# Optimization experiments

Measured on AMD Instinct MI355X. Metric: run time of the kernel, lower is better.

## Reference

```python
import jax, jax.numpy as jnp
import numpy as np

B, S, D_IN, D_HID, D_OUT, H = 2, 2048, 1024, 1024, 1024, 16
HD = D_HID // H  # head_dim = 64


def setup_inputs() -> dict:
    key = jax.random.key(0)
    ks = jax.random.split(key, 9)
    s_in = 1.0 / np.sqrt(D_IN)
    s_out = 1.0 / np.sqrt(D_OUT)
    return {
        "x": jax.random.normal(ks[0], (B, S, D_IN), dtype=jnp.float32),
        "Wq": jax.random.uniform(ks[1], (D_IN, D_HID), jnp.float32, -s_in, s_in),
        "bq": jax.random.uniform(ks[2], (D_HID,), jnp.float32, -s_in, s_in),
        "Wk": jax.random.uniform(ks[3], (D_IN, D_HID), jnp.float32, -s_in, s_in),
        "bk": jax.random.uniform(ks[4], (D_HID,), jnp.float32, -s_in, s_in),
        "Wv": jax.random.uniform(ks[5], (D_IN, D_OUT), jnp.float32, -s_in, s_in),
        "bv": jax.random.uniform(ks[6], (D_OUT,), jnp.float32, -s_in, s_in),
        "Wo": jax.random.uniform(ks[7], (D_OUT, D_OUT), jnp.float32, -s_out, s_out),
        "bo": jax.random.uniform(ks[8], (D_OUT,), jnp.float32, -s_out, s_out),
    }


def reference(x, Wq, bq, Wk, bk, Wv, bv, Wo, bo):
    b, s, _ = x.shape
    q = (x @ Wq + bq).reshape(b, s, H, HD)  # [B,S,H,HD]
    k = (x @ Wk + bk).reshape(b, s, H, HD)
    v = (x @ Wv + bv).reshape(b, s, H, HD)
    scores = jnp.einsum("bqhd,bkhd->bhqk", q, k) / jnp.sqrt(jnp.float32(HD))
    attn = jax.nn.softmax(scores, axis=-1)  # [B,H,S,S]
    ctx = jnp.einsum("bhqk,bkhd->bqhd", attn, v).reshape(b, s, D_HID)
    return ctx @ Wo + bo
```

## Files before the change

### kernel.cpp

```cpp
#include <hip/hip_runtime.h>
#include <stdint.h>

typedef __attribute__((ext_vector_type(8))) short short8v;
typedef __attribute__((ext_vector_type(4))) short short4v;
typedef __attribute__((ext_vector_type(4))) float float4v;
typedef __attribute__((ext_vector_type(4))) unsigned short ushort4v;
typedef __attribute__((ext_vector_type(4))) float floatvec4;
typedef __attribute__((ext_vector_type(2))) unsigned int uint2v;
typedef __attribute__((ext_vector_type(4))) unsigned int uint4v;

#define DEVI __device__ __forceinline__

DEVI unsigned short f2bf(float f) {
    unsigned int u = __builtin_bit_cast(unsigned int, f);
    u += 0x7FFFu + ((u >> 16) & 1u);
    return (unsigned short)(u >> 16);
}

DEVI unsigned int pk2bf(float a, float b) {
#if defined(__has_builtin) && __has_builtin(__builtin_amdgcn_cvt_pk_bf16_f32)
    auto r = __builtin_amdgcn_cvt_pk_bf16_f32(a, b);
    unsigned int u;
    __builtin_memcpy(&u, &r, 4);
    return u;
#else
    return (unsigned int)f2bf(a) | ((unsigned int)f2bf(b) << 16);
#endif
}

DEVI float ex2(float x) {
#if defined(__has_builtin) && __has_builtin(__builtin_amdgcn_exp2f)
    return __builtin_amdgcn_exp2f(x);
#else
    return __builtin_exp2f(x);
#endif
}

DEVI uint2v pl32swap(unsigned int d, unsigned int s) {
#if defined(__has_builtin) && __has_builtin(__builtin_amdgcn_permlane32_swap)
    return __builtin_amdgcn_permlane32_swap(d, s, false, false);
#else
    const int hi = (int)(threadIdx.x & 32);
    unsigned int dp = __shfl_xor(d, 32), sp = __shfl_xor(s, 32);
    return (uint2v){hi ? sp : d, hi ? s : dp};
#endif
}
DEVI uint2v pl16swap(unsigned int d, unsigned int s) {
#if defined(__has_builtin) && __has_builtin(__builtin_amdgcn_permlane16_swap)
    return __builtin_amdgcn_permlane16_swap(d, s, false, false);
#else
    const int lo = (int)(threadIdx.x & 16);
    unsigned int dp = __shfl_xor(d, 16), sp = __shfl_xor(s, 16);
    return (uint2v){lo ? sp : d, lo ? s : dp};
#endif
}

typedef __attribute__((address_space(1))) void GV;
typedef __attribute__((address_space(3))) void LV;
DEVI void gl2lds16(const void* g, void* l) {
    __builtin_amdgcn_global_load_lds((GV*)g, (LV*)l, 16, 0, 0);
}

__global__ void prep_kernel(const float* __restrict__ x, unsigned short* __restrict__ xb,
                            const float* __restrict__ W0, const float* __restrict__ W1,
                            const float* __restrict__ W2, const float* __restrict__ W3,
                            unsigned short* __restrict__ D0, unsigned short* __restrict__ D1,
                            unsigned short* __restrict__ D2, unsigned short* __restrict__ D3) {
    const int bid = blockIdx.x, tid = threadIdx.x;
    if (bid < 4096) {
        const int i = (bid * 256 + tid) * 4;
        const floatvec4 v = *(const floatvec4*)&x[i];
        ushort4v o;
#pragma unroll
        for (int r = 0; r < 4; r++) o[r] = f2bf(v[r]);
        *(ushort4v*)&xb[i] = o;
        return;
    }
    __shared__ float t[32][33];
    const int tcode = bid - 4096;
    const int z = tcode >> 10, rem = tcode & 1023;
    const int by = rem >> 5, bx = rem & 31;
    const int tx = tid & 31, ty = tid >> 5;
    const float* W = (z == 0) ? W0 : (z == 1) ? W1 : (z == 2) ? W2 : W3;
    unsigned short* D = (z == 0) ? D0 : (z == 1) ? D1 : (z == 2) ? D2 : D3;
#pragma unroll
    for (int i = 0; i < 4; i++)
        t[ty + i * 8][tx] = W[(size_t)(by * 32 + ty + i * 8) * 1024 + bx * 32 + tx];
    __syncthreads();
#pragma unroll
    for (int i = 0; i < 4; i++)
        D[(size_t)(bx * 32 + ty + i * 8) * 1024 + by * 32 + tx] = f2bf(t[tx][ty + i * 8]);
}

__global__ __launch_bounds__(256, 3) void qkv_gemm(
    const unsigned short* __restrict__ X, const unsigned short* __restrict__ Wt,
    const float* __restrict__ bq, const float* __restrict__ bk, const float* __restrict__ bv,
    unsigned short* __restrict__ qb, unsigned short* __restrict__ kb,
    unsigned short* __restrict__ vtb)
{
    __shared__ __align__(16) unsigned short As[128 * 64];
    __shared__ __align__(16) unsigned short Bs[128 * 64];
    const int tid = threadIdx.x, lane = tid & 63, wv = tid >> 6;
    const int quad = lane >> 4, l16 = lane & 15;
    const int w = blockIdx.x >> 3;
    const int n0 = (blockIdx.x & 7) * 128;
    const int row0 = blockIdx.y * 128;
    const unsigned short* Wsel = Wt + (size_t)w * (1024 * 1024);

    const int srow = lane >> 3;
    const int qsc = ((lane & 7) ^ (lane >> 3 & 7)) * 8;
    const int fsw = l16 & 7;
    const int wm = (wv >> 1) * 64, wn = (wv & 1) * 64;

    float4v acc[4][4];
#pragma unroll
    for (int i = 0; i < 4; i++)
#pragma unroll
        for (int j = 0; j < 4; j++) acc[i][j] = (float4v){0.f, 0.f, 0.f, 0.f};

    for (int k0 = 0; k0 < 1024; k0 += 64) {
        __syncthreads();
#pragma unroll
        for (int i = 0; i < 4; i++) {
            const int c = wv * 4 + i;
            gl2lds16(X + (size_t)(row0 + c * 8 + srow) * 1024 + k0 + qsc, As + c * 512);
            gl2lds16(Wsel + (size_t)(n0 + c * 8 + srow) * 1024 + k0 + qsc, Bs + c * 512);
        }
        __syncthreads();
#pragma unroll
        for (int kc = 0; kc < 2; kc++) {
            const int sl = (((kc * 4 + quad) ^ fsw) * 8);
            short8v a[4], b[4];
#pragma unroll
            for (int mt = 0; mt < 4; mt++)
                a[mt] = *(const short8v*)&As[(wm + mt * 16 + l16) * 64 + sl];
#pragma unroll
            for (int nt = 0; nt < 4; nt++)
                b[nt] = *(const short8v*)&Bs[(wn + nt * 16 + l16) * 64 + sl];
#pragma unroll
            for (int mt = 0; mt < 4; mt++)
#pragma unroll
                for (int nt = 0; nt < 4; nt++)
                    acc[mt][nt] = __builtin_amdgcn_mfma_f32_16x16x32_bf16(a[mt], b[nt], acc[mt][nt], 0, 0, 0);
        }
    }

    const float* bias = (w == 0) ? bq : (w == 1) ? bk : bv;
    const float scl = (w == 0) ? 0.18033688011112042f : 1.0f;
#pragma unroll
    for (int nt = 0; nt < 4; nt++) {
        const int col = n0 + wn + nt * 16 + l16;
        const float bb = bias[col];
        const int h = col >> 6, hd = col & 63;
#pragma unroll
        for (int mt = 0; mt < 4; mt++) {
            const int tok0 = row0 + wm + mt * 16 + quad * 4;
            const int b_ = tok0 >> 11, s0 = tok0 & 2047;
            if (w == 2) {
                ushort4v pk;
#pragma unroll
                for (int r = 0; r < 4; r++) pk[r] = f2bf(acc[mt][nt][r] + bb);
                *(ushort4v*)&vtb[(((size_t)b_ * 16 + h) * 64 + hd) * 2048 + s0] = pk;
            } else {
                unsigned short* dst = (w == 0) ? qb : kb;
#pragma unroll
                for (int r = 0; r < 4; r++)
                    dst[(((size_t)b_ * 16 + h) * 2048 + (s0 + r)) * 64 + hd] =
                        f2bf((acc[mt][nt][r] + bb) * scl);
            }
        }
    }
}

__global__ __launch_bounds__(256, 2) void attn_kernel(
    const unsigned short* __restrict__ qb, const unsigned short* __restrict__ kb,
    const unsigned short* __restrict__ vtb, unsigned short* __restrict__ ctxb)
{
    __shared__ __align__(16) unsigned short Kt[2 * 128 * 64];
    __shared__ __align__(16) unsigned short Vt[2 * 64 * 128];
    const int tid = threadIdx.x, lane = tid & 63, wv = tid >> 6;
    const int quad = lane >> 4, l16 = lane & 15;
    const int bh = blockIdx.x, qt = blockIdx.y;
    const size_t boff = (size_t)bh * (2048 * 64);
    const unsigned short* qp = qb + boff;
    const unsigned short* kp = kb + boff;
    const unsigned short* vp = vtb + boff;
    const int q0 = qt * 128 + wv * 32;

    short8v qf[2][2];
#pragma unroll
    for (int nt = 0; nt < 2; nt++)
#pragma unroll
        for (int kc = 0; kc < 2; kc++)
            qf[nt][kc] = *(const short8v*)&qp[(size_t)(q0 + nt * 16 + l16) * 64 + kc * 32 + quad * 8];

    float4v accO[2][4];
#pragma unroll
    for (int nt = 0; nt < 2; nt++)
#pragma unroll
        for (int ht = 0; ht < 4; ht++) accO[nt][ht] = (float4v){0.f, 0.f, 0.f, 0.f};
    float lsum[2] = {0.f, 0.f};

    const int krow = lane >> 3;
    const int kg = (lane & 7) ^ (lane >> 3);
    const int vrow = lane >> 4;
    const int rsw = l16 & 7;

    const int ktb0 = l16 * 64 + ((quad ^ rsw) * 8);
    const int ktb1 = l16 * 64 + (((4 + quad) ^ rsw) * 8);
    const int vrb = l16 * 128 + ((quad ^ (l16 & 3)) * 8);
    const int l12e = (l16 & 12) * 8;

    auto stage = [&](int kt0, int bn) {
        unsigned short* Kd = Kt + bn * (128 * 64);
        unsigned short* Vd = Vt + bn * (64 * 128);
#pragma unroll
        for (int i = 0; i < 4; i++) {
            const int c = wv * 4 + i;
            gl2lds16(kp + (size_t)(kt0 + c * 8 + krow) * 64 + kg * 8, Kd + c * 512);
            const int vr = c * 4 + vrow;
            const int vg = (lane & 15) ^ (vr & 15);
            gl2lds16(vp + (size_t)vr * 2048 + kt0 + vg * 8, Vd + c * 512);
        }
    };

    stage(0, 0);
    __syncthreads();

    for (int t = 0; t < 16; ++t) {
        if (t < 15) stage((t + 1) * 128, (t & 1) ^ 1);
        const unsigned short* Kc = Kt + (t & 1) * (128 * 64);
        const unsigned short* Vc = Vt + (t & 1) * (64 * 128);

        unsigned int pkr[8][2][2];
#pragma unroll
        for (int mt = 0; mt < 8; mt++) {
            const short8v a0 = *(const short8v*)&Kc[ktb0 + mt * 1024];
            const short8v a1 = *(const short8v*)&Kc[ktb1 + mt * 1024];
#pragma unroll
            for (int nt = 0; nt < 2; nt++) {
                float4v z = (float4v){0.f, 0.f, 0.f, 0.f};
                z = __builtin_amdgcn_mfma_f32_16x16x32_bf16(a0, qf[nt][0], z, 0, 0, 0);
                z = __builtin_amdgcn_mfma_f32_16x16x32_bf16(a1, qf[nt][1], z, 0, 0, 0);
                const float p0 = ex2(z[0]), p1 = ex2(z[1]);
                const float p2 = ex2(z[2]), p3 = ex2(z[3]);
                lsum[nt] += (p0 + p1) + (p2 + p3);
                pkr[mt][nt][0] = pk2bf(p0, p1);
                pkr[mt][nt][1] = pk2bf(p2, p3);
            }
        }

#pragma unroll
        for (int kc = 0; kc < 4; kc++) {
            const int roff = (kc * 32) ^ l12e;
            short8v bvv[4];
#pragma unroll
            for (int ht = 0; ht < 4; ht++)
                bvv[ht] = *(const short8v*)&Vc[vrb + roff + ht * 2048];
#pragma unroll
            for (int nt = 0; nt < 2; nt++) {
                const uint2v s0 = pl32swap(pkr[2 * kc][nt][0], pkr[2 * kc + 1][nt][0]);
                const uint2v s1 = pl32swap(pkr[2 * kc][nt][1], pkr[2 * kc + 1][nt][1]);
                const uint2v t0 = pl16swap(s0.x, s0.y);
                const uint2v t1 = pl16swap(s1.x, s1.y);
                const uint4v fu = (uint4v){t0.x, t1.x, t0.y, t1.y};
                const short8v ap = __builtin_bit_cast(short8v, fu);
#pragma unroll
                for (int ht = 0; ht < 4; ht++)
                    accO[nt][ht] = __builtin_amdgcn_mfma_f32_16x16x32_bf16(ap, bvv[ht], accO[nt][ht], 0, 0, 0);
            }
        }
        __syncthreads();
    }

#pragma unroll
    for (int nt = 0; nt < 2; nt++) {
        lsum[nt] += __shfl_xor(lsum[nt], 16);
        lsum[nt] += __shfl_xor(lsum[nt], 32);
    }

    const int b_ = bh >> 4, h = bh & 15;
#pragma unroll
    for (int nt = 0; nt < 2; nt++)
#pragma unroll
        for (int r = 0; r < 4; r++) {
            const int s = q0 + nt * 16 + quad * 4 + r;
            const float inv = 1.0f / __shfl(lsum[nt], quad * 4 + r);
#pragma unroll
            for (int ht = 0; ht < 4; ht++) {
                const int hd = ht * 16 + l16;
                ctxb[((size_t)(b_ * 2048 + s)) * 1024 + h * 64 + hd] = f2bf(accO[nt][ht][r] * inv);
            }
        }
}

__global__ __launch_bounds__(256, 2) void out_gemm(
    const unsigned short* __restrict__ ctx, const unsigned short* __restrict__ Wot,
    const float* __restrict__ bo, float* __restrict__ out)
{
    __shared__ __align__(16) unsigned short As[128 * 64];
    __shared__ __align__(16) unsigned short Bs[64 * 64];
    const int tid = threadIdx.x, lane = tid & 63, wv = tid >> 6;
    const int quad = lane >> 4, l16 = lane & 15;
    const int n0 = blockIdx.x * 64;
    const int row0 = blockIdx.y * 128;

    const int srow = lane >> 3;
    const int qsc = ((lane & 7) ^ (lane >> 3 & 7)) * 8;
    const int fsw = l16 & 7;
    const int wm = (wv & 1) * 64, wn = (wv >> 1) * 32;

    float4v acc[4][2];
#pragma unroll
    for (int i = 0; i < 4; i++)
#pragma unroll
        for (int j = 0; j < 2; j++) acc[i][j] = (float4v){0.f, 0.f, 0.f, 0.f};

    for (int k0 = 0; k0 < 1024; k0 += 64) {
        __syncthreads();
#pragma unroll
        for (int i = 0; i < 6; i++) {
            const int c = wv * 6 + i;
            if (c < 16)
                gl2lds16(ctx + (size_t)(row0 + c * 8 + srow) * 1024 + k0 + qsc, As + c * 512);
            else
                gl2lds16(Wot + (size_t)(n0 + (c - 16) * 8 + srow) * 1024 + k0 + qsc,
                         Bs + (c - 16) * 512);
        }
        __syncthreads();
#pragma unroll
        for (int kc = 0; kc < 2; kc++) {
            const int sl = (((kc * 4 + quad) ^ fsw) * 8);
            short8v a[4], b[2];
#pragma unroll
            for (int mt = 0; mt < 4; mt++)
                a[mt] = *(const short8v*)&As[(wm + mt * 16 + l16) * 64 + sl];
#pragma unroll
            for (int nt = 0; nt < 2; nt++)
                b[nt] = *(const short8v*)&Bs[(wn + nt * 16 + l16) * 64 + sl];
#pragma unroll
            for (int mt = 0; mt < 4; mt++)
#pragma unroll
                for (int nt = 0; nt < 2; nt++)
                    acc[mt][nt] = __builtin_amdgcn_mfma_f32_16x16x32_bf16(a[mt], b[nt], acc[mt][nt], 0, 0, 0);
        }
    }

#pragma unroll
    for (int nt = 0; nt < 2; nt++) {
        const int col = n0 + wn + nt * 16 + l16;
        const float bb = bo[col];
#pragma unroll
        for (int mt = 0; mt < 4; mt++) {
            const int tok0 = row0 + wm + mt * 16 + quad * 4;
#pragma unroll
            for (int r = 0; r < 4; r++)
                out[(size_t)(tok0 + r) * 1024 + col] = acc[mt][nt][r] + bb;
        }
    }
}

extern "C" void kernel_launch(void* const* d_in, const int* in_sizes, int n_in,
                              void* d_out, int out_size, void* d_ws, size_t ws_size,
                              hipStream_t stream) {
    const float* x  = (const float*)d_in[0];
    const float* Wq = (const float*)d_in[1];
    const float* bq = (const float*)d_in[2];
    const float* Wk = (const float*)d_in[3];
    const float* bk = (const float*)d_in[4];
    const float* Wv = (const float*)d_in[5];
    const float* bv = (const float*)d_in[6];
    const float* Wo = (const float*)d_in[7];
    const float* bo = (const float*)d_in[8];
    float* out = (float*)d_out;

    char* ws = (char*)d_ws;
    unsigned short* xb   = (unsigned short*)(ws);
    unsigned short* qbuf = (unsigned short*)(ws + (8u << 20));
    unsigned short* kbuf = (unsigned short*)(ws + (16u << 20));
    unsigned short* vtb  = (unsigned short*)(ws + (24u << 20));
    unsigned short* wt   = (unsigned short*)(ws + (32u << 20));
    unsigned short* wot  = (unsigned short*)(ws + (38u << 20));

    prep_kernel<<<8192, 256, 0, stream>>>(x, xb, Wq, Wk, Wv, Wo,
                                          wt, wt + (1u << 20), wt + (2u << 20), wot);
    qkv_gemm<<<dim3(24, 32), 256, 0, stream>>>(xb, wt, bq, bk, bv, qbuf, kbuf, vtb);
    attn_kernel<<<dim3(32, 16), 256, 0, stream>>>(qbuf, kbuf, vtb, xb );
    out_gemm<<<dim3(16, 32), 256, 0, stream>>>(xb, wot, bo, out);
}
```

Baseline: 193.9 us.

## Split attention query tile across 8 waves of 16 rows each

The attention kernel now launches 512 threads (8 waves) per block, and each wave handles 16 query rows instead of 32. Staging of K/V tiles is spread across twice as many waves. The aim is more waves in flight and fewer registers per wave, to hide latency better. In exchange, each K/V fragment read from LDS now feeds only one query tile, so LDS reads per MFMA double. The launch bound also requests 4 blocks per CU, which may force register limits.

```diff
diff --git a/kernel.cpp b/kernel.cpp
--- a/kernel.cpp
+++ b/kernel.cpp
@@ -172,7 +172,7 @@
     }
 }
 
-__global__ __launch_bounds__(256, 2) void attn_kernel(
+__global__ __launch_bounds__(512, 4) void attn_kernel(
     const unsigned short* __restrict__ qb, const unsigned short* __restrict__ kb,
     const unsigned short* __restrict__ vtb, unsigned short* __restrict__ ctxb)
 {
@@ -185,21 +185,17 @@
     const unsigned short* qp = qb + boff;
     const unsigned short* kp = kb + boff;
     const unsigned short* vp = vtb + boff;
-    const int q0 = qt * 128 + wv * 32;
-
-    short8v qf[2][2];
-#pragma unroll
-    for (int nt = 0; nt < 2; nt++)
-#pragma unroll
-        for (int kc = 0; kc < 2; kc++)
-            qf[nt][kc] = *(const short8v*)&qp[(size_t)(q0 + nt * 16 + l16) * 64 + kc * 32 + quad * 8];
-
-    float4v accO[2][4];
-#pragma unroll
-    for (int nt = 0; nt < 2; nt++)
-#pragma unroll
-        for (int ht = 0; ht < 4; ht++) accO[nt][ht] = (float4v){0.f, 0.f, 0.f, 0.f};
-    float lsum[2] = {0.f, 0.f};
+    const int q0 = qt * 128 + wv * 16;
+
+    short8v qf[2];
+#pragma unroll
+    for (int kc = 0; kc < 2; kc++)
+        qf[kc] = *(const short8v*)&qp[(size_t)(q0 + l16) * 64 + kc * 32 + quad * 8];
+
+    float4v accO[4];
+#pragma unroll
+    for (int ht = 0; ht < 4; ht++) accO[ht] = (float4v){0.f, 0.f, 0.f, 0.f};
+    float lsum = 0.f;
 
     const int krow = lane >> 3;
     const int kg = (lane & 7) ^ (lane >> 3);
@@ -215,8 +211,8 @@
         unsigned short* Kd = Kt + bn * (128 * 64);
         unsigned short* Vd = Vt + bn * (64 * 128);
 #pragma unroll
-        for (int i = 0; i < 4; i++) {
-            const int c = wv * 4 + i;
+        for (int i = 0; i < 2; i++) {
+            const int c = wv * 2 + i;
             gl2lds16(kp + (size_t)(kt0 + c * 8 + krow) * 64 + kg * 8, Kd + c * 512);
             const int vr = c * 4 + vrow;
             const int vg = (lane & 15) ^ (vr & 15);
@@ -232,22 +228,19 @@
         const unsigned short* Kc = Kt + (t & 1) * (128 * 64);
         const unsigned short* Vc = Vt + (t & 1) * (64 * 128);
 
-        unsigned int pkr[8][2][2];
+        unsigned int pkr[8][2];
 #pragma unroll
         for (int mt = 0; mt < 8; mt++) {
             const short8v a0 = *(const short8v*)&Kc[ktb0 + mt * 1024];
             const short8v a1 = *(const short8v*)&Kc[ktb1 + mt * 1024];
-#pragma unroll
-            for (int nt = 0; nt < 2; nt++) {
-                float4v z = (float4v){0.f, 0.f, 0.f, 0.f};
-                z = __builtin_amdgcn_mfma_f32_16x16x32_bf16(a0, qf[nt][0], z, 0, 0, 0);
-                z = __builtin_amdgcn_mfma_f32_16x16x32_bf16(a1, qf[nt][1], z, 0, 0, 0);
-                const float p0 = ex2(z[0]), p1 = ex2(z[1]);
-                const float p2 = ex2(z[2]), p3 = ex2(z[3]);
-                lsum[nt] += (p0 + p1) + (p2 + p3);
-                pkr[mt][nt][0] = pk2bf(p0, p1);
-                pkr[mt][nt][1] = pk2bf(p2, p3);
-            }
+            float4v z = (float4v){0.f, 0.f, 0.f, 0.f};
+            z = __builtin_amdgcn_mfma_f32_16x16x32_bf16(a0, qf[0], z, 0, 0, 0);
+            z = __builtin_amdgcn_mfma_f32_16x16x32_bf16(a1, qf[1], z, 0, 0, 0);
+            const float p0 = ex2(z[0]), p1 = ex2(z[1]);
+            const float p2 = ex2(z[2]), p3 = ex2(z[3]);
+            lsum += (p0 + p1) + (p2 + p3);
+            pkr[mt][0] = pk2bf(p0, p1);
+            pkr[mt][1] = pk2bf(p2, p3);
         }
 
 #pragma unroll
@@ -257,41 +250,33 @@
 #pragma unroll
             for (int ht = 0; ht < 4; ht++)
                 bvv[ht] = *(const short8v*)&Vc[vrb + roff + ht * 2048];
-#pragma unroll
-            for (int nt = 0; nt < 2; nt++) {
-                const uint2v s0 = pl32swap(pkr[2 * kc][nt][0], pkr[2 * kc + 1][nt][0]);
-                const uint2v s1 = pl32swap(pkr[2 * kc][nt][1], pkr[2 * kc + 1][nt][1]);
-                const uint2v t0 = pl16swap(s0.x, s0.y);
-                const uint2v t1 = pl16swap(s1.x, s1.y);
-                const uint4v fu = (uint4v){t0.x, t1.x, t0.y, t1.y};
-                const short8v ap = __builtin_bit_cast(short8v, fu);
-#pragma unroll
-                for (int ht = 0; ht < 4; ht++)
-                    accO[nt][ht] = __builtin_amdgcn_mfma_f32_16x16x32_bf16(ap, bvv[ht], accO[nt][ht], 0, 0, 0);
-            }
-        }
-        __syncthreads();
-    }
-
-#pragma unroll
-    for (int nt = 0; nt < 2; nt++) {
-        lsum[nt] += __shfl_xor(lsum[nt], 16);
-        lsum[nt] += __shfl_xor(lsum[nt], 32);
-    }
+            const uint2v s0 = pl32swap(pkr[2 * kc][0], pkr[2 * kc + 1][0]);
+            const uint2v s1 = pl32swap(pkr[2 * kc][1], pkr[2 * kc + 1][1]);
+            const uint2v t0 = pl16swap(s0.x, s0.y);
+            const uint2v t1 = pl16swap(s1.x, s1.y);
+            const uint4v fu = (uint4v){t0.x, t1.x, t0.y, t1.y};
+            const short8v ap = __builtin_bit_cast(short8v, fu);
+#pragma unroll
+            for (int ht = 0; ht < 4; ht++)
+                accO[ht] = __builtin_amdgcn_mfma_f32_16x16x32_bf16(ap, bvv[ht], accO[ht], 0, 0, 0);
+        }
+        __syncthreads();
+    }
+
+    lsum += __shfl_xor(lsum, 16);
+    lsum += __shfl_xor(lsum, 32);
 
     const int b_ = bh >> 4, h = bh & 15;
 #pragma unroll
-    for (int nt = 0; nt < 2; nt++)
-#pragma unroll
-        for (int r = 0; r < 4; r++) {
-            const int s = q0 + nt * 16 + quad * 4 + r;
-            const float inv = 1.0f / __shfl(lsum[nt], quad * 4 + r);
-#pragma unroll
-            for (int ht = 0; ht < 4; ht++) {
-                const int hd = ht * 16 + l16;
-                ctxb[((size_t)(b_ * 2048 + s)) * 1024 + h * 64 + hd] = f2bf(accO[nt][ht][r] * inv);
-            }
-        }
+    for (int r = 0; r < 4; r++) {
+        const int s = q0 + quad * 4 + r;
+        const float inv = 1.0f / __shfl(lsum, quad * 4 + r);
+#pragma unroll
+        for (int ht = 0; ht < 4; ht++) {
+            const int hd = ht * 16 + l16;
+            ctxb[((size_t)(b_ * 2048 + s)) * 1024 + h * 64 + hd] = f2bf(accO[ht][r] * inv);
+        }
+    }
 }
 
 __global__ __launch_bounds__(256, 2) void out_gemm(
@@ -385,6 +370,6 @@
     prep_kernel<<<8192, 256, 0, stream>>>(x, xb, Wq, Wk, Wv, Wo,
                                           wt, wt + (1u << 20), wt + (2u << 20), wot);
     qkv_gemm<<<dim3(24, 32), 256, 0, stream>>>(xb, wt, bq, bk, bv, qbuf, kbuf, vtb);
-    attn_kernel<<<dim3(32, 16), 256, 0, stream>>>(qbuf, kbuf, vtb, xb );
+    attn_kernel<<<dim3(32, 16), 512, 0, stream>>>(qbuf, kbuf, vtb, xb );
     out_gemm<<<dim3(16, 32), 256, 0, stream>>>(xb, wot, bo, out);
 }
```

New measurement: 194.7 us. No clear change (+0.4%).

## Load K/V fragments directly from global memory instead of LDS staging

Applied to the files above, without the earlier changes.

Removes the double-buffered LDS staging of K and V tiles, along with the per-iteration barrier. Each wave now reads its MFMA operand fragments straight from global memory (relying on the L2/L1 caches), and s_setprio raises wave priority around the PV MFMAs. This eliminates LDS traffic and block synchronisation. In exchange, every wave redundantly fetches the same K/V data from global memory with no prefetch, which exposes load latency and raises cache bandwidth demand.

```diff
diff --git a/kernel.cpp b/kernel.cpp
--- a/kernel.cpp
+++ b/kernel.cpp
@@ -176,8 +176,6 @@
     const unsigned short* __restrict__ qb, const unsigned short* __restrict__ kb,
     const unsigned short* __restrict__ vtb, unsigned short* __restrict__ ctxb)
 {
-    __shared__ __align__(16) unsigned short Kt[2 * 128 * 64];
-    __shared__ __align__(16) unsigned short Vt[2 * 64 * 128];
     const int tid = threadIdx.x, lane = tid & 63, wv = tid >> 6;
     const int quad = lane >> 4, l16 = lane & 15;
     const int bh = blockIdx.x, qt = blockIdx.y;
@@ -201,42 +199,16 @@
         for (int ht = 0; ht < 4; ht++) accO[nt][ht] = (float4v){0.f, 0.f, 0.f, 0.f};
     float lsum[2] = {0.f, 0.f};
 
-    const int krow = lane >> 3;
-    const int kg = (lane & 7) ^ (lane >> 3);
-    const int vrow = lane >> 4;
-    const int rsw = l16 & 7;
-
-    const int ktb0 = l16 * 64 + ((quad ^ rsw) * 8);
-    const int ktb1 = l16 * 64 + (((4 + quad) ^ rsw) * 8);
-    const int vrb = l16 * 128 + ((quad ^ (l16 & 3)) * 8);
-    const int l12e = (l16 & 12) * 8;
-
-    auto stage = [&](int kt0, int bn) {
-        unsigned short* Kd = Kt + bn * (128 * 64);
-        unsigned short* Vd = Vt + bn * (64 * 128);
-#pragma unroll
-        for (int i = 0; i < 4; i++) {
-            const int c = wv * 4 + i;
-            gl2lds16(kp + (size_t)(kt0 + c * 8 + krow) * 64 + kg * 8, Kd + c * 512);
-            const int vr = c * 4 + vrow;
-            const int vg = (lane & 15) ^ (vr & 15);
-            gl2lds16(vp + (size_t)vr * 2048 + kt0 + vg * 8, Vd + c * 512);
-        }
-    };
-
-    stage(0, 0);
-    __syncthreads();
-
-    for (int t = 0; t < 16; ++t) {
-        if (t < 15) stage((t + 1) * 128, (t & 1) ^ 1);
-        const unsigned short* Kc = Kt + (t & 1) * (128 * 64);
-        const unsigned short* Vc = Vt + (t & 1) * (64 * 128);
-
+    const unsigned short* kfb = kp + (size_t)l16 * 64 + quad * 8;
+    const unsigned short* vfb = vp + (size_t)l16 * 2048 + quad * 8;
+
+    for (int kt0 = 0; kt0 < 2048; kt0 += 128) {
         unsigned int pkr[8][2][2];
 #pragma unroll
         for (int mt = 0; mt < 8; mt++) {
-            const short8v a0 = *(const short8v*)&Kc[ktb0 + mt * 1024];
-            const short8v a1 = *(const short8v*)&Kc[ktb1 + mt * 1024];
+            const unsigned short* kr = kfb + (size_t)(kt0 + mt * 16) * 64;
+            const short8v a0 = *(const short8v*)(kr);
+            const short8v a1 = *(const short8v*)(kr + 32);
 #pragma unroll
             for (int nt = 0; nt < 2; nt++) {
                 float4v z = (float4v){0.f, 0.f, 0.f, 0.f};
@@ -252,11 +224,10 @@
 
 #pragma unroll
         for (int kc = 0; kc < 4; kc++) {
-            const int roff = (kc * 32) ^ l12e;
             short8v bvv[4];
 #pragma unroll
             for (int ht = 0; ht < 4; ht++)
-                bvv[ht] = *(const short8v*)&Vc[vrb + roff + ht * 2048];
+                bvv[ht] = *(const short8v*)(vfb + (size_t)(ht * 16) * 2048 + kt0 + kc * 32);
 #pragma unroll
             for (int nt = 0; nt < 2; nt++) {
                 const uint2v s0 = pl32swap(pkr[2 * kc][nt][0], pkr[2 * kc + 1][nt][0]);
@@ -265,12 +236,13 @@
                 const uint2v t1 = pl16swap(s1.x, s1.y);
                 const uint4v fu = (uint4v){t0.x, t1.x, t0.y, t1.y};
                 const short8v ap = __builtin_bit_cast(short8v, fu);
+                __builtin_amdgcn_s_setprio(1);
 #pragma unroll
                 for (int ht = 0; ht < 4; ht++)
                     accO[nt][ht] = __builtin_amdgcn_mfma_f32_16x16x32_bf16(ap, bvv[ht], accO[nt][ht], 0, 0, 0);
+                __builtin_amdgcn_s_setprio(0);
             }
         }
-        __syncthreads();
     }
 
 #pragma unroll
```

Measured after the change: 255.6 us. +31.8%, slower.
